# Performance work log

Measured on AMD Instinct MI355X. Metric: run time of the kernel, lower is better.

The kernel has to match this reference:

```python
import jax, jax.numpy as jnp
import numpy as np

B, K, E, L, H, ENS = 32768, 5, 16, 128, 3, 3

def setup_inputs() -> dict:
    key = jax.random.key(0)
    ks = jax.random.split(key, 16)
    w = lambda i, shape: (jax.random.normal(ks[i], shape, jnp.float32) * 0.05)
    return {
        "z": jax.random.normal(ks[0], (B, L), jnp.float32),
        "anchors": jax.random.normal(ks[1], (B, K, 2), jnp.float32),
        # anchor_embed MLP: Linear(2,E) -> ReLU -> Linear(E,E)
        "W1": w(2, (E, 2)), "b1": w(3, (E,)),
        "W2": w(4, (E, E)), "b2": w(5, (E,)),
        # LSTMCell(E, L): gates order i,f,g,o
        "W_ih": w(6, (4 * L, E)), "W_hh": w(7, (4 * L, L)),
        "b_ih": w(8, (4 * L,)), "b_hh": w(9, (4 * L,)),
        # progress head Linear(L,1)
        "Wp": w(10, (1, L)), "bp": w(11, (1,)),
        # risk ensemble: ENS stacked Linear(L,1)
        "Wr": w(12, (ENS, L)), "br": w(13, (ENS,)),
    }

def reference(z, anchors, W1, b1, W2, b2, W_ih, W_hh, b_ih, b_hh, Wp, bp, Wr, br):
    Bc, Kc, _ = anchors.shape
    # anchor embedding MLP (B,K,2) -> (B,K,E)
    emb = jnp.maximum(anchors @ W1.T + b1, 0.0) @ W2.T + b2
    inp = emb.reshape(Bc * Kc, -1)                      # (B*K, E)
    h = jnp.broadcast_to(z[:, None, :], (Bc, Kc, z.shape[-1])).reshape(Bc * Kc, -1)
    c = jnp.zeros_like(h)
    x_proj = inp @ W_ih.T + b_ih                        # input projection constant over steps
    for _ in range(H):  # fixed small rollout horizon
        gates = x_proj + h @ W_hh.T + b_hh              # (B*K, 4L)
        i_g, f_g, g_g, o_g = jnp.split(gates, 4, axis=-1)
        i_g = jax.nn.sigmoid(i_g)
        f_g = jax.nn.sigmoid(f_g)
        g_g = jnp.tanh(g_g)
        o_g = jax.nn.sigmoid(o_g)
        c = f_g * c + i_g * g_g
        h = o_g * jnp.tanh(c)
    h = h.reshape(Bc, Kc, -1)                           # (B,K,L)
    progress = (h @ Wp.T + bp)[..., 0]                  # (B,K)
    risks = jnp.einsum('bkl,el->ebk', h, Wr) + br[:, None, None]  # (ENS,B,K)
    risk_mean = risks.mean(axis=0)
    unc = jnp.var(jax.nn.sigmoid(risks), axis=0, ddof=1)  # torch .var is unbiased
    return risk_mean, progress, unc, risks
```

## Files before the change

kernel.cpp:

```cpp
#include <hip/hip_runtime.h>

#define BN 32768
#define KN 5
#define LN 128
#define HN 3
#define ROWS (BN*KN)
#define BK ROWS
#define MT 64
#define TILES (ROWS/MT)
#define WGS 512
#define TPW (TILES/WGS)
#define THREADS 512
#define ASTR 168
#define LOG2E 1.44269504089f

using bf16x8 = __attribute__((ext_vector_type(8))) __bf16;
using bf16x2 = __attribute__((ext_vector_type(2))) __bf16;
using f32x4  = __attribute__((ext_vector_type(4))) float;
using u16x8  = __attribute__((ext_vector_type(8))) unsigned short;

__device__ inline unsigned short f2bf(float x) {
    union { float f; unsigned u; } v; v.f = x;
    unsigned r = v.u + 0x7FFFu + ((v.u >> 16) & 1u);
    return (unsigned short)(r >> 16);
}
#if __has_builtin(__builtin_amdgcn_cvt_pk_bf16_f32)
__device__ inline unsigned short f2bf_fast(float x) {
    union { bf16x2 v; unsigned short us[2]; } u;
    u.v = __builtin_amdgcn_cvt_pk_bf16_f32(x, x);
    return u.us[0];
}
#else
__device__ inline unsigned short f2bf_fast(float x) { return f2bf(x); }
#endif
__device__ inline float bf2f(unsigned short b) {
    union { unsigned u; float f; } v; v.u = ((unsigned)b) << 16; return v.f;
}
__device__ inline float sigm(float x) {
    return __builtin_amdgcn_rcpf(1.0f + __builtin_amdgcn_exp2f(-LOG2E * x));
}
__device__ inline f32x4 splat4(float x) { f32x4 r; r[0]=x; r[1]=x; r[2]=x; r[3]=x; return r; }

__global__ __launch_bounds__(THREADS, 2)
void wahead_kernel(const float* __restrict__ z,   const float* __restrict__ anchors,
                   const float* __restrict__ W1,  const float* __restrict__ b1,
                   const float* __restrict__ W2,  const float* __restrict__ b2,
                   const float* __restrict__ Wih, const float* __restrict__ Whh,
                   const float* __restrict__ bih, const float* __restrict__ bhh,
                   const float* __restrict__ Wp,  const float* __restrict__ bp,
                   const float* __restrict__ Wr,  const float* __restrict__ br,
                   float* __restrict__ out)
{
    __shared__ unsigned short sA[2 * MT * ASTR];
    __shared__ float sW1[32], sb1[16], sW2[16 * 17], sb2[16], sWp[128], sWr[384];

    const int tid  = threadIdx.x;
    const int wv   = tid >> 6;
    const int lane = tid & 63;
    const int quad = lane >> 4;
    const int cc   = lane & 15;

    if (tid < 32)  sW1[tid] = W1[tid];
    if (tid < 16)  { sb1[tid] = b1[tid]; sb2[tid] = b2[tid]; }
    if (tid < 256) sW2[(tid >> 4) * 17 + (tid & 15)] = W2[tid];
    if (tid < 128) sWp[tid] = Wp[tid];
    if (tid < 384) sWr[tid] = Wr[tid];

    bf16x8 Bf[4][5];
    float  biasv[4];
    #pragma unroll
    for (int t = 0; t < 4; ++t) {
        const float sc = (t == 2) ? (2.0f * LOG2E) : (-LOG2E);
        const int n = t * 128 + wv * 16 + cc;
        biasv[t] = sc * (bih[n] + bhh[n]);
        #pragma unroll
        for (int kt = 0; kt < 5; ++kt) {
            const int k0 = kt * 32 + quad * 8;
            float v[8];
            if (k0 < 16) {
                const float4 p0 = *reinterpret_cast<const float4*>(Wih + n * 16 + k0);
                const float4 p1 = *reinterpret_cast<const float4*>(Wih + n * 16 + k0 + 4);
                v[0]=p0.x; v[1]=p0.y; v[2]=p0.z; v[3]=p0.w;
                v[4]=p1.x; v[5]=p1.y; v[6]=p1.z; v[7]=p1.w;
            } else if (k0 < 144) {
                const float4 p0 = *reinterpret_cast<const float4*>(Whh + n * 128 + (k0 - 16));
                const float4 p1 = *reinterpret_cast<const float4*>(Whh + n * 128 + (k0 - 16) + 4);
                v[0]=p0.x; v[1]=p0.y; v[2]=p0.z; v[3]=p0.w;
                v[4]=p1.x; v[5]=p1.y; v[6]=p1.z; v[7]=p1.w;
            } else {
                #pragma unroll
                for (int j = 0; j < 8; ++j) v[j] = 0.0f;
            }
            union { bf16x8 bv; unsigned short us[8]; } pk;
            #pragma unroll
            for (int j = 0; j < 8; ++j) pk.us[j] = f2bf(sc * v[j]);
            Bf[t][kt] = pk.bv;
        }
    }

    const float bpv = bp[0];
    const float br0 = br[0], br1 = br[1], br2 = br[2];

    __syncthreads();

    const int erow = tid >> 3;
    const int esub = tid & 7;

    #pragma unroll 1
    for (int ti = 0; ti < TPW; ++ti) {
        const int tile = blockIdx.x * TPW + ti;
        const int r0g  = tile * MT;

        {
            const int gr = r0g + erow;
            const float ax = anchors[gr * 2], ay = anchors[gr * 2 + 1];
            const int e0 = esub * 2;
            float a0 = sb2[e0], a1 = sb2[e0 + 1];
            #pragma unroll
            for (int hh = 0; hh < 16; ++hh) {
                float pre = fmaf(sW1[hh * 2], ax, fmaf(sW1[hh * 2 + 1], ay, sb1[hh]));
                pre = fmaxf(pre, 0.0f);
                a0 = fmaf(pre, sW2[e0 * 17 + hh], a0);
                a1 = fmaf(pre, sW2[(e0 + 1) * 17 + hh], a1);
            }
            const unsigned short b0 = f2bf(a0), b1v = f2bf(a1);
            #pragma unroll
            for (int bufi = 0; bufi < 2; ++bufi) {
                unsigned short* row = &sA[bufi * MT * ASTR + erow * ASTR];
                row[e0]       = b0;  row[e0 + 1]       = b1v;
                row[144 + e0] = 0;   row[144 + e0 + 1] = 0;
            }
            const unsigned b_idx = (unsigned)gr / 5u;
            const float4* zp = reinterpret_cast<const float4*>(z + (size_t)b_idx * 128 + esub * 16);
            const float4 z0 = zp[0], z1 = zp[1], z2 = zp[2], z3 = zp[3];
            union { u16x8 v; unsigned short us[8]; } w0, w1;
            w0.us[0]=f2bf(z0.x); w0.us[1]=f2bf(z0.y); w0.us[2]=f2bf(z0.z); w0.us[3]=f2bf(z0.w);
            w0.us[4]=f2bf(z1.x); w0.us[5]=f2bf(z1.y); w0.us[6]=f2bf(z1.z); w0.us[7]=f2bf(z1.w);
            w1.us[0]=f2bf(z2.x); w1.us[1]=f2bf(z2.y); w1.us[2]=f2bf(z2.z); w1.us[3]=f2bf(z2.w);
            w1.us[4]=f2bf(z3.x); w1.us[5]=f2bf(z3.y); w1.us[6]=f2bf(z3.z); w1.us[7]=f2bf(z3.w);
            unsigned short* hrow = &sA[erow * ASTR + 16 + esub * 16];
            *reinterpret_cast<u16x8*>(hrow)     = w0.v;
            *reinterpret_cast<u16x8*>(hrow + 8) = w1.v;
        }

        float cst[16];
        #pragma unroll
        for (int e = 0; e < 16; ++e) cst[e] = 0.0f;

        #pragma unroll
        for (int s = 0; s < HN; ++s) {
            const int cur = s & 1;
            const int nxt = cur ^ 1;
            __syncthreads();

            f32x4 acc[4][4];
            #pragma unroll
            for (int mt = 0; mt < 4; ++mt)
                #pragma unroll
                for (int t = 0; t < 4; ++t)
                    acc[mt][t] = splat4(biasv[t]);

            bf16x8 af[2][5];
            #pragma unroll
            for (int kt = 0; kt < 5; ++kt)
                af[0][kt] = *reinterpret_cast<const bf16x8*>(
                    &sA[cur * MT * ASTR + cc * ASTR + kt * 32 + quad * 8]);
            #pragma unroll
            for (int mt = 0; mt < 4; ++mt) {
                const int pb = mt & 1;
                if (mt < 3) {
                    #pragma unroll
                    for (int kt = 0; kt < 5; ++kt)
                        af[pb ^ 1][kt] = *reinterpret_cast<const bf16x8*>(
                            &sA[cur * MT * ASTR + ((mt + 1) * 16 + cc) * ASTR + kt * 32 + quad * 8]);
                }
                #pragma unroll
                for (int kt = 0; kt < 5; ++kt)
                    #pragma unroll
                    for (int t = 0; t < 4; ++t)
                        acc[mt][t] = __builtin_amdgcn_mfma_f32_16x16x32_bf16(
                            af[pb][kt], Bf[t][kt], acc[mt][t], 0, 0, 0);
            }

            const int lcol = wv * 16 + cc;
            #pragma unroll
            for (int e = 0; e < 16; ++e) {
                const int mt = e >> 2, r = e & 3;
                const float Ei = __builtin_amdgcn_exp2f(acc[mt][0][r]);
                const float Ef = __builtin_amdgcn_exp2f(acc[mt][1][r]);
                const float Eg = __builtin_amdgcn_exp2f(acc[mt][2][r]);
                const float Eo = __builtin_amdgcn_exp2f(acc[mt][3][r]);
                const float t1  = (1.0f + Ei) * (1.0f + Eg);
                const float ef1 = 1.0f + Ef;
                const float t3  = (Eg - 1.0f) * ef1;
                const float num = fmaf(cst[e], t1, t3);
                const float cn  = num * __builtin_amdgcn_rcpf(t1 * ef1);
                cst[e] = cn;
                const float Ec = __builtin_amdgcn_exp2f(2.0f * LOG2E * cn);
                const float hn = (Ec - 1.0f) *
                    __builtin_amdgcn_rcpf((1.0f + Eo) * (1.0f + Ec));
                const int m = mt * 16 + quad * 4 + r;
                sA[nxt * MT * ASTR + m * ASTR + 16 + lcol] = f2bf_fast(hn);
            }
        }

        __syncthreads();

        {
            const int row = tid >> 3;
            const int j   = tid & 7;
            const unsigned short* hrow = &sA[1 * MT * ASTR + row * ASTR + 16 + j * 16];
            const u16x8 h0 = *reinterpret_cast<const u16x8*>(hrow);
            const u16x8 h1 = *reinterpret_cast<const u16x8*>(hrow + 8);
            float p = 0.f, q0 = 0.f, q1 = 0.f, q2 = 0.f;
            #pragma unroll
            for (int u = 0; u < 16; ++u) {
                const int l = j * 16 + u;
                const float hv = bf2f(u < 8 ? h0[u] : h1[u - 8]);
                p  = fmaf(hv, sWp[l], p);
                q0 = fmaf(hv, sWr[l], q0);
                q1 = fmaf(hv, sWr[128 + l], q1);
                q2 = fmaf(hv, sWr[256 + l], q2);
            }
            #pragma unroll
            for (int m = 1; m < 8; m <<= 1) {
                p  += __shfl_xor(p,  m, 64);
                q0 += __shfl_xor(q0, m, 64);
                q1 += __shfl_xor(q1, m, 64);
                q2 += __shfl_xor(q2, m, 64);
            }
            if (j == 0) {
                const int gr = r0g + row;
                const float prog  = p + bpv;
                const float rr0 = q0 + br0, rr1 = q1 + br1, rr2 = q2 + br2;
                const float rmean = (rr0 + rr1 + rr2) * (1.0f / 3.0f);
                const float s0 = sigm(rr0), s1 = sigm(rr1), s2 = sigm(rr2);
                const float sm = (s0 + s1 + s2) * (1.0f / 3.0f);
                const float d0 = s0 - sm, d1 = s1 - sm, d2 = s2 - sm;
                const float unc = (d0 * d0 + d1 * d1 + d2 * d2) * 0.5f;
                out[gr]          = rmean;
                out[BK + gr]     = prog;
                out[2 * BK + gr] = unc;
                out[3 * BK + gr] = rr0;
                out[4 * BK + gr] = rr1;
                out[5 * BK + gr] = rr2;
            }
        }
    }
}

extern "C" void kernel_launch(void* const* d_in, const int* in_sizes, int n_in,
                              void* d_out, int out_size, void* d_ws, size_t ws_size,
                              hipStream_t stream) {
    const float* z       = (const float*)d_in[0];
    const float* anchors = (const float*)d_in[1];
    const float* W1      = (const float*)d_in[2];
    const float* b1      = (const float*)d_in[3];
    const float* W2      = (const float*)d_in[4];
    const float* b2      = (const float*)d_in[5];
    const float* Wih     = (const float*)d_in[6];
    const float* Whh     = (const float*)d_in[7];
    const float* bih     = (const float*)d_in[8];
    const float* bhh     = (const float*)d_in[9];
    const float* Wp      = (const float*)d_in[10];
    const float* bp      = (const float*)d_in[11];
    const float* Wr      = (const float*)d_in[12];
    const float* br      = (const float*)d_in[13];

    hipLaunchKernelGGL(wahead_kernel, dim3(WGS), dim3(THREADS), 0, stream,
                       z, anchors, W1, b1, W2, b2, Wih, Whh, bih, bhh,
                       Wp, bp, Wr, br, (float*)d_out);
}
```

Measured before the change: 213.0 us.

## Split gate GEMM across 16 waves and exchange gates through LDS

Restructures the LSTM tile processing. Tiles shrink to 32 rows and workgroups grow to 1024 threads, and each wave now computes 32 gate columns of one gate type instead of all four gates for 16 columns. Gate pre-activations go through a new LDS buffer so the elementwise cell update can be spread over all threads, with an extra barrier per step. This cuts per-thread register pressure (fewer B fragments and accumulators) to raise parallelism, at the cost of extra LDS traffic, an extra sync per step and a wider shuffle reduction.

```diff
diff --git a/kernel.cpp b/kernel.cpp
--- a/kernel.cpp
+++ b/kernel.cpp
@@ -6,18 +6,20 @@
 #define HN 3
 #define ROWS (BN*KN)
 #define BK ROWS
-#define MT 64
+#define MT 32
 #define TILES (ROWS/MT)
 #define WGS 512
 #define TPW (TILES/WGS)
-#define THREADS 512
+#define THREADS 1024
 #define ASTR 168
+#define GSTR 132
 #define LOG2E 1.44269504089f
 
 using bf16x8 = __attribute__((ext_vector_type(8))) __bf16;
 using bf16x2 = __attribute__((ext_vector_type(2))) __bf16;
 using f32x4  = __attribute__((ext_vector_type(4))) float;
 using u16x8  = __attribute__((ext_vector_type(8))) unsigned short;
+using u16x4  = __attribute__((ext_vector_type(4))) unsigned short;
 
 __device__ inline unsigned short f2bf(float x) {
     union { float f; unsigned u; } v; v.f = x;
@@ -41,7 +43,7 @@
 }
 __device__ inline f32x4 splat4(float x) { f32x4 r; r[0]=x; r[1]=x; r[2]=x; r[3]=x; return r; }
 
-__global__ __launch_bounds__(THREADS, 2)
+__global__ __launch_bounds__(THREADS)
 void wahead_kernel(const float* __restrict__ z,   const float* __restrict__ anchors,
                    const float* __restrict__ W1,  const float* __restrict__ b1,
                    const float* __restrict__ W2,  const float* __restrict__ b2,
@@ -52,13 +54,16 @@
                    float* __restrict__ out)
 {
     __shared__ unsigned short sA[2 * MT * ASTR];
+    __shared__ float sG[4 * MT * GSTR];
     __shared__ float sW1[32], sb1[16], sW2[16 * 17], sb2[16], sWp[128], sWr[384];
 
     const int tid  = threadIdx.x;
-    const int wv   = tid >> 6;
+    const int v    = tid >> 6;
     const int lane = tid & 63;
     const int quad = lane >> 4;
     const int cc   = lane & 15;
+    const int tg   = v >> 2;
+    const int l0   = 32 * (v & 3);
 
     if (tid < 32)  sW1[tid] = W1[tid];
     if (tid < 16)  { sb1[tid] = b1[tid]; sb2[tid] = b2[tid]; }
@@ -66,35 +71,35 @@
     if (tid < 128) sWp[tid] = Wp[tid];
     if (tid < 384) sWr[tid] = Wr[tid];
 
-    bf16x8 Bf[4][5];
-    float  biasv[4];
+    const float sc = (tg == 2) ? (2.0f * LOG2E) : (-LOG2E);
+    bf16x8 Bf[2][5];
+    float  biasv[2];
     #pragma unroll
-    for (int t = 0; t < 4; ++t) {
-        const float sc = (t == 2) ? (2.0f * LOG2E) : (-LOG2E);
-        const int n = t * 128 + wv * 16 + cc;
-        biasv[t] = sc * (bih[n] + bhh[n]);
+    for (int nt = 0; nt < 2; ++nt) {
+        const int n = 32 * v + nt * 16 + cc;
+        biasv[nt] = sc * (bih[n] + bhh[n]);
         #pragma unroll
         for (int kt = 0; kt < 5; ++kt) {
             const int k0 = kt * 32 + quad * 8;
-            float v[8];
+            float w[8];
             if (k0 < 16) {
                 const float4 p0 = *reinterpret_cast<const float4*>(Wih + n * 16 + k0);
                 const float4 p1 = *reinterpret_cast<const float4*>(Wih + n * 16 + k0 + 4);
-                v[0]=p0.x; v[1]=p0.y; v[2]=p0.z; v[3]=p0.w;
-                v[4]=p1.x; v[5]=p1.y; v[6]=p1.z; v[7]=p1.w;
+                w[0]=p0.x; w[1]=p0.y; w[2]=p0.z; w[3]=p0.w;
+                w[4]=p1.x; w[5]=p1.y; w[6]=p1.z; w[7]=p1.w;
             } else if (k0 < 144) {
                 const float4 p0 = *reinterpret_cast<const float4*>(Whh + n * 128 + (k0 - 16));
                 const float4 p1 = *reinterpret_cast<const float4*>(Whh + n * 128 + (k0 - 16) + 4);
-                v[0]=p0.x; v[1]=p0.y; v[2]=p0.z; v[3]=p0.w;
-                v[4]=p1.x; v[5]=p1.y; v[6]=p1.z; v[7]=p1.w;
+                w[0]=p0.x; w[1]=p0.y; w[2]=p0.z; w[3]=p0.w;
+                w[4]=p1.x; w[5]=p1.y; w[6]=p1.z; w[7]=p1.w;
             } else {
                 #pragma unroll
-                for (int j = 0; j < 8; ++j) v[j] = 0.0f;
+                for (int j = 0; j < 8; ++j) w[j] = 0.0f;
             }
             union { bf16x8 bv; unsigned short us[8]; } pk;
             #pragma unroll
-            for (int j = 0; j < 8; ++j) pk.us[j] = f2bf(sc * v[j]);
-            Bf[t][kt] = pk.bv;
+            for (int j = 0; j < 8; ++j) pk.us[j] = f2bf(sc * w[j]);
+            Bf[nt][kt] = pk.bv;
         }
     }
 
@@ -103,8 +108,8 @@
 
     __syncthreads();
 
-    const int erow = tid >> 3;
-    const int esub = tid & 7;
+    const int erow = tid >> 5;
+    const int ej   = tid & 31;
 
     #pragma unroll 1
     for (int ti = 0; ti < TPW; ++ti) {
@@ -113,39 +118,29 @@
 
         {
             const int gr = r0g + erow;
-            const float ax = anchors[gr * 2], ay = anchors[gr * 2 + 1];
-            const int e0 = esub * 2;
-            float a0 = sb2[e0], a1 = sb2[e0 + 1];
-            #pragma unroll
-            for (int hh = 0; hh < 16; ++hh) {
-                float pre = fmaf(sW1[hh * 2], ax, fmaf(sW1[hh * 2 + 1], ay, sb1[hh]));
-                pre = fmaxf(pre, 0.0f);
-                a0 = fmaf(pre, sW2[e0 * 17 + hh], a0);
-                a1 = fmaf(pre, sW2[(e0 + 1) * 17 + hh], a1);
-            }
-            const unsigned short b0 = f2bf(a0), b1v = f2bf(a1);
-            #pragma unroll
-            for (int bufi = 0; bufi < 2; ++bufi) {
-                unsigned short* row = &sA[bufi * MT * ASTR + erow * ASTR];
-                row[e0]       = b0;  row[e0 + 1]       = b1v;
-                row[144 + e0] = 0;   row[144 + e0 + 1] = 0;
+            if (ej < 16) {
+                const float ax = anchors[gr * 2], ay = anchors[gr * 2 + 1];
+                float acc_e = sb2[ej];
+                #pragma unroll
+                for (int hh = 0; hh < 16; ++hh) {
+                    float pre = fmaf(sW1[hh * 2], ax, fmaf(sW1[hh * 2 + 1], ay, sb1[hh]));
+                    pre = fmaxf(pre, 0.0f);
+                    acc_e = fmaf(pre, sW2[ej * 17 + hh], acc_e);
+                }
+                const unsigned short eb = f2bf(acc_e);
+                sA[0 * MT * ASTR + erow * ASTR + ej] = eb;
+                sA[1 * MT * ASTR + erow * ASTR + ej] = eb;
+                sA[0 * MT * ASTR + erow * ASTR + 144 + ej] = 0;
+                sA[1 * MT * ASTR + erow * ASTR + 144 + ej] = 0;
             }
             const unsigned b_idx = (unsigned)gr / 5u;
-            const float4* zp = reinterpret_cast<const float4*>(z + (size_t)b_idx * 128 + esub * 16);
-            const float4 z0 = zp[0], z1 = zp[1], z2 = zp[2], z3 = zp[3];
-            union { u16x8 v; unsigned short us[8]; } w0, w1;
-            w0.us[0]=f2bf(z0.x); w0.us[1]=f2bf(z0.y); w0.us[2]=f2bf(z0.z); w0.us[3]=f2bf(z0.w);
-            w0.us[4]=f2bf(z1.x); w0.us[5]=f2bf(z1.y); w0.us[6]=f2bf(z1.z); w0.us[7]=f2bf(z1.w);
-            w1.us[0]=f2bf(z2.x); w1.us[1]=f2bf(z2.y); w1.us[2]=f2bf(z2.z); w1.us[3]=f2bf(z2.w);
-            w1.us[4]=f2bf(z3.x); w1.us[5]=f2bf(z3.y); w1.us[6]=f2bf(z3.z); w1.us[7]=f2bf(z3.w);
-            unsigned short* hrow = &sA[erow * ASTR + 16 + esub * 16];
-            *reinterpret_cast<u16x8*>(hrow)     = w0.v;
-            *reinterpret_cast<u16x8*>(hrow + 8) = w1.v;
-        }
-
-        float cst[16];
-        #pragma unroll
-        for (int e = 0; e < 16; ++e) cst[e] = 0.0f;
+            const float4 zv = *reinterpret_cast<const float4*>(z + (size_t)b_idx * 128 + ej * 4);
+            union { u16x4 v4; unsigned short us[4]; } zz;
+            zz.us[0]=f2bf(zv.x); zz.us[1]=f2bf(zv.y); zz.us[2]=f2bf(zv.z); zz.us[3]=f2bf(zv.w);
+            *reinterpret_cast<u16x4*>(&sA[erow * ASTR + 16 + ej * 4]) = zz.v4;
+        }
+
+        float cst[4] = {0, 0, 0, 0};
 
         #pragma unroll
         for (int s = 0; s < HN; ++s) {
@@ -153,83 +148,75 @@
             const int nxt = cur ^ 1;
             __syncthreads();
 
-            f32x4 acc[4][4];
-            #pragma unroll
-            for (int mt = 0; mt < 4; ++mt)
-                #pragma unroll
-                for (int t = 0; t < 4; ++t)
-                    acc[mt][t] = splat4(biasv[t]);
-
-            bf16x8 af[2][5];
-            #pragma unroll
-            for (int kt = 0; kt < 5; ++kt)
-                af[0][kt] = *reinterpret_cast<const bf16x8*>(
-                    &sA[cur * MT * ASTR + cc * ASTR + kt * 32 + quad * 8]);
-            #pragma unroll
-            for (int mt = 0; mt < 4; ++mt) {
-                const int pb = mt & 1;
-                if (mt < 3) {
+            #pragma unroll
+            for (int mt = 0; mt < 2; ++mt) {
+                bf16x8 a[5];
+                #pragma unroll
+                for (int kt = 0; kt < 5; ++kt)
+                    a[kt] = *reinterpret_cast<const bf16x8*>(
+                        &sA[cur * MT * ASTR + (mt * 16 + cc) * ASTR + kt * 32 + quad * 8]);
+                #pragma unroll
+                for (int nt = 0; nt < 2; ++nt) {
+                    f32x4 g = splat4(biasv[nt]);
                     #pragma unroll
                     for (int kt = 0; kt < 5; ++kt)
-                        af[pb ^ 1][kt] = *reinterpret_cast<const bf16x8*>(
-                            &sA[cur * MT * ASTR + ((mt + 1) * 16 + cc) * ASTR + kt * 32 + quad * 8]);
+                        g = __builtin_amdgcn_mfma_f32_16x16x32_bf16(a[kt], Bf[nt][kt], g, 0, 0, 0);
+                    const int base = (tg * 32 + mt * 16 + quad * 4) * GSTR + l0 + nt * 16 + cc;
+                    #pragma unroll
+                    for (int r = 0; r < 4; ++r) sG[base + r * GSTR] = g[r];
                 }
-                #pragma unroll
-                for (int kt = 0; kt < 5; ++kt)
-                    #pragma unroll
-                    for (int t = 0; t < 4; ++t)
-                        acc[mt][t] = __builtin_amdgcn_mfma_f32_16x16x32_bf16(
-                            af[pb][kt], Bf[t][kt], acc[mt][t], 0, 0, 0);
-            }
-
-            const int lcol = wv * 16 + cc;
-            #pragma unroll
-            for (int e = 0; e < 16; ++e) {
-                const int mt = e >> 2, r = e & 3;
-                const float Ei = __builtin_amdgcn_exp2f(acc[mt][0][r]);
-                const float Ef = __builtin_amdgcn_exp2f(acc[mt][1][r]);
-                const float Eg = __builtin_amdgcn_exp2f(acc[mt][2][r]);
-                const float Eo = __builtin_amdgcn_exp2f(acc[mt][3][r]);
+            }
+
+            __syncthreads();
+
+            #pragma unroll
+            for (int e = 0; e < 4; ++e) {
+                const int row = 2 * v + (e >> 1);
+                const int l   = lane + 64 * (e & 1);
+                const float gi = sG[(0 * MT + row) * GSTR + l];
+                const float gf = sG[(1 * MT + row) * GSTR + l];
+                const float gg = sG[(2 * MT + row) * GSTR + l];
+                const float go = sG[(3 * MT + row) * GSTR + l];
+                const float Ei = __builtin_amdgcn_exp2f(gi);
+                const float Ef = __builtin_amdgcn_exp2f(gf);
+                const float Eg = __builtin_amdgcn_exp2f(gg);
+                const float Eo = __builtin_amdgcn_exp2f(go);
                 const float t1  = (1.0f + Ei) * (1.0f + Eg);
                 const float ef1 = 1.0f + Ef;
-                const float t3  = (Eg - 1.0f) * ef1;
-                const float num = fmaf(cst[e], t1, t3);
+                const float num = fmaf(cst[e], t1, (Eg - 1.0f) * ef1);
                 const float cn  = num * __builtin_amdgcn_rcpf(t1 * ef1);
                 cst[e] = cn;
                 const float Ec = __builtin_amdgcn_exp2f(2.0f * LOG2E * cn);
                 const float hn = (Ec - 1.0f) *
                     __builtin_amdgcn_rcpf((1.0f + Eo) * (1.0f + Ec));
-                const int m = mt * 16 + quad * 4 + r;
-                sA[nxt * MT * ASTR + m * ASTR + 16 + lcol] = f2bf_fast(hn);
+                sA[nxt * MT * ASTR + row * ASTR + 16 + l] = f2bf_fast(hn);
             }
         }
 
         __syncthreads();
 
         {
-            const int row = tid >> 3;
-            const int j   = tid & 7;
-            const unsigned short* hrow = &sA[1 * MT * ASTR + row * ASTR + 16 + j * 16];
-            const u16x8 h0 = *reinterpret_cast<const u16x8*>(hrow);
-            const u16x8 h1 = *reinterpret_cast<const u16x8*>(hrow + 8);
+            const int row = erow;
+            const u16x4 hv4 = *reinterpret_cast<const u16x4*>(
+                &sA[1 * MT * ASTR + row * ASTR + 16 + ej * 4]);
             float p = 0.f, q0 = 0.f, q1 = 0.f, q2 = 0.f;
             #pragma unroll
-            for (int u = 0; u < 16; ++u) {
-                const int l = j * 16 + u;
-                const float hv = bf2f(u < 8 ? h0[u] : h1[u - 8]);
+            for (int u = 0; u < 4; ++u) {
+                const int l = ej * 4 + u;
+                const float hv = bf2f(hv4[u]);
                 p  = fmaf(hv, sWp[l], p);
                 q0 = fmaf(hv, sWr[l], q0);
                 q1 = fmaf(hv, sWr[128 + l], q1);
                 q2 = fmaf(hv, sWr[256 + l], q2);
             }
             #pragma unroll
-            for (int m = 1; m < 8; m <<= 1) {
+            for (int m = 1; m < 32; m <<= 1) {
                 p  += __shfl_xor(p,  m, 64);
                 q0 += __shfl_xor(q0, m, 64);
                 q1 += __shfl_xor(q1, m, 64);
                 q2 += __shfl_xor(q2, m, 64);
             }
-            if (j == 0) {
+            if (ej == 0) {
                 const int gr = r0g + row;
                 const float prog  = p + bpv;
                 const float rr0 = q0 + br0, rr1 = q1 + br1, rr2 = q2 + br2;
@@ -248,6 +235,7 @@
         }
     }
 }
+
 
 extern "C" void kernel_launch(void* const* d_in, const int* in_sizes, int n_in,
                               void* d_out, int out_size, void* d_ws, size_t ws_size,
```

Measured after the change: 279.7 us. 1.31x slower.

## Split tiles into two half-pipelines interleaving MFMA with LSTM pointwise and epilogue

Applied to the files above, without the earlier changes.

Each 64-row tile is split into two 32-row halves that run software-pipelined. The MFMA gate product for one half is issued while the exp/rcp pointwise LSTM update of the other half runs, so the matrix and transcendental units can overlap. The final hidden state goes to a separate LDS buffer, which lets the previous tile's head and epilogue run during the next tile's first step. The cost is extra barriers per tile, more LDS, and higher register pressure from two live accumulator sets.

```diff
diff --git a/kernel.cpp b/kernel.cpp
--- a/kernel.cpp
+++ b/kernel.cpp
@@ -12,6 +12,7 @@
 #define TPW (TILES/WGS)
 #define THREADS 512
 #define ASTR 168
+#define FSTR 136
 #define LOG2E 1.44269504089f
 
 using bf16x8 = __attribute__((ext_vector_type(8))) __bf16;
@@ -52,6 +53,7 @@
                    float* __restrict__ out)
 {
     __shared__ unsigned short sA[2 * MT * ASTR];
+    __shared__ unsigned short sF[MT * FSTR];
     __shared__ float sW1[32], sb1[16], sW2[16 * 17], sb2[16], sWp[128], sWr[384];
 
     const int tid  = threadIdx.x;
@@ -101,152 +103,173 @@
     const float bpv = bp[0];
     const float br0 = br[0], br1 = br[1], br2 = br[2];
 
+    f32x4 acc0[2][4], acc1[2][4];
+    float cst0[8], cst1[8];
+
+    auto do_mfma = [&](f32x4 (&acc)[2][4], int pipe, int buf) {
+        #pragma unroll
+        for (int mt = 0; mt < 2; ++mt)
+            #pragma unroll
+            for (int t = 0; t < 4; ++t) acc[mt][t] = splat4(biasv[t]);
+        #pragma unroll
+        for (int mt = 0; mt < 2; ++mt) {
+            const int row = pipe * 32 + mt * 16 + cc;
+            bf16x8 a[5];
+            #pragma unroll
+            for (int kt = 0; kt < 5; ++kt)
+                a[kt] = *reinterpret_cast<const bf16x8*>(
+                    &sA[buf * MT * ASTR + row * ASTR + kt * 32 + quad * 8]);
+            #pragma unroll
+            for (int kt = 0; kt < 5; ++kt)
+                #pragma unroll
+                for (int t = 0; t < 4; ++t)
+                    acc[mt][t] = __builtin_amdgcn_mfma_f32_16x16x32_bf16(
+                        a[kt], Bf[t][kt], acc[mt][t], 0, 0, 0);
+        }
+    };
+
+    auto do_pw = [&](f32x4 (&acc)[2][4], float (&cst)[8], int pipe, int dstbuf,
+                     bool final_h) {
+        const int lcol = wv * 16 + cc;
+        #pragma unroll
+        for (int e = 0; e < 8; ++e) {
+            const int mt = e >> 2, r = e & 3;
+            const float Ei = __builtin_amdgcn_exp2f(acc[mt][0][r]);
+            const float Ef = __builtin_amdgcn_exp2f(acc[mt][1][r]);
+            const float Eg = __builtin_amdgcn_exp2f(acc[mt][2][r]);
+            const float Eo = __builtin_amdgcn_exp2f(acc[mt][3][r]);
+            const float t1  = (1.0f + Ei) * (1.0f + Eg);
+            const float ef1 = 1.0f + Ef;
+            const float num = fmaf(cst[e], t1, (Eg - 1.0f) * ef1);
+            const float cn  = num * __builtin_amdgcn_rcpf(t1 * ef1);
+            cst[e] = cn;
+            const float Ec = __builtin_amdgcn_exp2f(2.0f * LOG2E * cn);
+            const float hn = (Ec - 1.0f) *
+                __builtin_amdgcn_rcpf((1.0f + Eo) * (1.0f + Ec));
+            const int m = pipe * 32 + mt * 16 + quad * 4 + r;
+            if (final_h) sF[m * FSTR + lcol] = f2bf_fast(hn);
+            else         sA[dstbuf * MT * ASTR + m * ASTR + 16 + lcol] = f2bf_fast(hn);
+        }
+    };
+
+    auto do_stage = [&](int r0g) {
+        const int erow = tid >> 3, esub = tid & 7;
+        const int gr = r0g + erow;
+        const float ax = anchors[gr * 2], ay = anchors[gr * 2 + 1];
+        const unsigned b_idx = (unsigned)gr / 5u;
+        const float4* zp = reinterpret_cast<const float4*>(z + (size_t)b_idx * 128 + esub * 16);
+        const float4 z0 = zp[0], z1 = zp[1], z2 = zp[2], z3 = zp[3];
+        const int e0 = esub * 2;
+        float a0 = sb2[e0], a1 = sb2[e0 + 1];
+        #pragma unroll
+        for (int hh = 0; hh < 16; ++hh) {
+            float pre = fmaf(sW1[hh * 2], ax, fmaf(sW1[hh * 2 + 1], ay, sb1[hh]));
+            pre = fmaxf(pre, 0.0f);
+            a0 = fmaf(pre, sW2[e0 * 17 + hh], a0);
+            a1 = fmaf(pre, sW2[(e0 + 1) * 17 + hh], a1);
+        }
+        const unsigned short b0 = f2bf(a0), b1v = f2bf(a1);
+        #pragma unroll
+        for (int bufi = 0; bufi < 2; ++bufi) {
+            unsigned short* row = &sA[bufi * MT * ASTR + erow * ASTR];
+            row[e0]       = b0;  row[e0 + 1]       = b1v;
+            row[144 + e0] = 0;   row[144 + e0 + 1] = 0;
+        }
+        union { u16x8 v; unsigned short us[8]; } w0, w1;
+        w0.us[0]=f2bf(z0.x); w0.us[1]=f2bf(z0.y); w0.us[2]=f2bf(z0.z); w0.us[3]=f2bf(z0.w);
+        w0.us[4]=f2bf(z1.x); w0.us[5]=f2bf(z1.y); w0.us[6]=f2bf(z1.z); w0.us[7]=f2bf(z1.w);
+        w1.us[0]=f2bf(z2.x); w1.us[1]=f2bf(z2.y); w1.us[2]=f2bf(z2.z); w1.us[3]=f2bf(z2.w);
+        w1.us[4]=f2bf(z3.x); w1.us[5]=f2bf(z3.y); w1.us[6]=f2bf(z3.z); w1.us[7]=f2bf(z3.w);
+        unsigned short* hrow = &sA[erow * ASTR + 16 + esub * 16];
+        *reinterpret_cast<u16x8*>(hrow)     = w0.v;
+        *reinterpret_cast<u16x8*>(hrow + 8) = w1.v;
+    };
+
+    auto do_epi = [&](int r0g) {
+        const int row = tid >> 3, j = tid & 7;
+        const unsigned short* hrow = &sF[row * FSTR + j * 16];
+        const u16x8 h0 = *reinterpret_cast<const u16x8*>(hrow);
+        const u16x8 h1 = *reinterpret_cast<const u16x8*>(hrow + 8);
+        float p = 0.f, q0 = 0.f, q1 = 0.f, q2 = 0.f;
+        #pragma unroll
+        for (int u = 0; u < 16; ++u) {
+            const int l = j * 16 + u;
+            const float hv = bf2f(u < 8 ? h0[u] : h1[u - 8]);
+            p  = fmaf(hv, sWp[l], p);
+            q0 = fmaf(hv, sWr[l], q0);
+            q1 = fmaf(hv, sWr[128 + l], q1);
+            q2 = fmaf(hv, sWr[256 + l], q2);
+        }
+        #pragma unroll
+        for (int m = 1; m < 8; m <<= 1) {
+            p  += __shfl_xor(p,  m, 64);
+            q0 += __shfl_xor(q0, m, 64);
+            q1 += __shfl_xor(q1, m, 64);
+            q2 += __shfl_xor(q2, m, 64);
+        }
+        if (j == 0) {
+            const int gr = r0g + row;
+            const float prog  = p + bpv;
+            const float rr0 = q0 + br0, rr1 = q1 + br1, rr2 = q2 + br2;
+            const float rmean = (rr0 + rr1 + rr2) * (1.0f / 3.0f);
+            const float s0 = sigm(rr0), s1 = sigm(rr1), s2 = sigm(rr2);
+            const float sm = (s0 + s1 + s2) * (1.0f / 3.0f);
+            const float d0 = s0 - sm, d1 = s1 - sm, d2 = s2 - sm;
+            const float unc = (d0 * d0 + d1 * d1 + d2 * d2) * 0.5f;
+            out[gr]          = rmean;
+            out[BK + gr]     = prog;
+            out[2 * BK + gr] = unc;
+            out[3 * BK + gr] = rr0;
+            out[4 * BK + gr] = rr1;
+            out[5 * BK + gr] = rr2;
+        }
+    };
+
     __syncthreads();
 
-    const int erow = tid >> 3;
-    const int esub = tid & 7;
+    int prev_r0g = 0;
+    bool have_prev = false;
 
     #pragma unroll 1
     for (int ti = 0; ti < TPW; ++ti) {
-        const int tile = blockIdx.x * TPW + ti;
-        const int r0g  = tile * MT;
-
-        {
-            const int gr = r0g + erow;
-            const float ax = anchors[gr * 2], ay = anchors[gr * 2 + 1];
-            const int e0 = esub * 2;
-            float a0 = sb2[e0], a1 = sb2[e0 + 1];
-            #pragma unroll
-            for (int hh = 0; hh < 16; ++hh) {
-                float pre = fmaf(sW1[hh * 2], ax, fmaf(sW1[hh * 2 + 1], ay, sb1[hh]));
-                pre = fmaxf(pre, 0.0f);
-                a0 = fmaf(pre, sW2[e0 * 17 + hh], a0);
-                a1 = fmaf(pre, sW2[(e0 + 1) * 17 + hh], a1);
-            }
-            const unsigned short b0 = f2bf(a0), b1v = f2bf(a1);
-            #pragma unroll
-            for (int bufi = 0; bufi < 2; ++bufi) {
-                unsigned short* row = &sA[bufi * MT * ASTR + erow * ASTR];
-                row[e0]       = b0;  row[e0 + 1]       = b1v;
-                row[144 + e0] = 0;   row[144 + e0 + 1] = 0;
-            }
-            const unsigned b_idx = (unsigned)gr / 5u;
-            const float4* zp = reinterpret_cast<const float4*>(z + (size_t)b_idx * 128 + esub * 16);
-            const float4 z0 = zp[0], z1 = zp[1], z2 = zp[2], z3 = zp[3];
-            union { u16x8 v; unsigned short us[8]; } w0, w1;
-            w0.us[0]=f2bf(z0.x); w0.us[1]=f2bf(z0.y); w0.us[2]=f2bf(z0.z); w0.us[3]=f2bf(z0.w);
-            w0.us[4]=f2bf(z1.x); w0.us[5]=f2bf(z1.y); w0.us[6]=f2bf(z1.z); w0.us[7]=f2bf(z1.w);
-            w1.us[0]=f2bf(z2.x); w1.us[1]=f2bf(z2.y); w1.us[2]=f2bf(z2.z); w1.us[3]=f2bf(z2.w);
-            w1.us[4]=f2bf(z3.x); w1.us[5]=f2bf(z3.y); w1.us[6]=f2bf(z3.z); w1.us[7]=f2bf(z3.w);
-            unsigned short* hrow = &sA[erow * ASTR + 16 + esub * 16];
-            *reinterpret_cast<u16x8*>(hrow)     = w0.v;
-            *reinterpret_cast<u16x8*>(hrow + 8) = w1.v;
-        }
-
-        float cst[16];
-        #pragma unroll
-        for (int e = 0; e < 16; ++e) cst[e] = 0.0f;
-
-        #pragma unroll
-        for (int s = 0; s < HN; ++s) {
-            const int cur = s & 1;
-            const int nxt = cur ^ 1;
-            __syncthreads();
-
-            f32x4 acc[4][4];
-            #pragma unroll
-            for (int mt = 0; mt < 4; ++mt)
-                #pragma unroll
-                for (int t = 0; t < 4; ++t)
-                    acc[mt][t] = splat4(biasv[t]);
-
-            bf16x8 af[2][5];
-            #pragma unroll
-            for (int kt = 0; kt < 5; ++kt)
-                af[0][kt] = *reinterpret_cast<const bf16x8*>(
-                    &sA[cur * MT * ASTR + cc * ASTR + kt * 32 + quad * 8]);
-            #pragma unroll
-            for (int mt = 0; mt < 4; ++mt) {
-                const int pb = mt & 1;
-                if (mt < 3) {
-                    #pragma unroll
-                    for (int kt = 0; kt < 5; ++kt)
-                        af[pb ^ 1][kt] = *reinterpret_cast<const bf16x8*>(
-                            &sA[cur * MT * ASTR + ((mt + 1) * 16 + cc) * ASTR + kt * 32 + quad * 8]);
-                }
-                #pragma unroll
-                for (int kt = 0; kt < 5; ++kt)
-                    #pragma unroll
-                    for (int t = 0; t < 4; ++t)
-                        acc[mt][t] = __builtin_amdgcn_mfma_f32_16x16x32_bf16(
-                            af[pb][kt], Bf[t][kt], acc[mt][t], 0, 0, 0);
-            }
-
-            const int lcol = wv * 16 + cc;
-            #pragma unroll
-            for (int e = 0; e < 16; ++e) {
-                const int mt = e >> 2, r = e & 3;
-                const float Ei = __builtin_amdgcn_exp2f(acc[mt][0][r]);
-                const float Ef = __builtin_amdgcn_exp2f(acc[mt][1][r]);
-                const float Eg = __builtin_amdgcn_exp2f(acc[mt][2][r]);
-                const float Eo = __builtin_amdgcn_exp2f(acc[mt][3][r]);
-                const float t1  = (1.0f + Ei) * (1.0f + Eg);
-                const float ef1 = 1.0f + Ef;
-                const float t3  = (Eg - 1.0f) * ef1;
-                const float num = fmaf(cst[e], t1, t3);
-                const float cn  = num * __builtin_amdgcn_rcpf(t1 * ef1);
-                cst[e] = cn;
-                const float Ec = __builtin_amdgcn_exp2f(2.0f * LOG2E * cn);
-                const float hn = (Ec - 1.0f) *
-                    __builtin_amdgcn_rcpf((1.0f + Eo) * (1.0f + Ec));
-                const int m = mt * 16 + quad * 4 + r;
-                sA[nxt * MT * ASTR + m * ASTR + 16 + lcol] = f2bf_fast(hn);
-            }
-        }
-
-        __syncthreads();
-
-        {
-            const int row = tid >> 3;
-            const int j   = tid & 7;
-            const unsigned short* hrow = &sA[1 * MT * ASTR + row * ASTR + 16 + j * 16];
-            const u16x8 h0 = *reinterpret_cast<const u16x8*>(hrow);
-            const u16x8 h1 = *reinterpret_cast<const u16x8*>(hrow + 8);
-            float p = 0.f, q0 = 0.f, q1 = 0.f, q2 = 0.f;
-            #pragma unroll
-            for (int u = 0; u < 16; ++u) {
-                const int l = j * 16 + u;
-                const float hv = bf2f(u < 8 ? h0[u] : h1[u - 8]);
-                p  = fmaf(hv, sWp[l], p);
-                q0 = fmaf(hv, sWr[l], q0);
-                q1 = fmaf(hv, sWr[128 + l], q1);
-                q2 = fmaf(hv, sWr[256 + l], q2);
-            }
-            #pragma unroll
-            for (int m = 1; m < 8; m <<= 1) {
-                p  += __shfl_xor(p,  m, 64);
-                q0 += __shfl_xor(q0, m, 64);
-                q1 += __shfl_xor(q1, m, 64);
-                q2 += __shfl_xor(q2, m, 64);
-            }
-            if (j == 0) {
-                const int gr = r0g + row;
-                const float prog  = p + bpv;
-                const float rr0 = q0 + br0, rr1 = q1 + br1, rr2 = q2 + br2;
-                const float rmean = (rr0 + rr1 + rr2) * (1.0f / 3.0f);
-                const float s0 = sigm(rr0), s1 = sigm(rr1), s2 = sigm(rr2);
-                const float sm = (s0 + s1 + s2) * (1.0f / 3.0f);
-                const float d0 = s0 - sm, d1 = s1 - sm, d2 = s2 - sm;
-                const float unc = (d0 * d0 + d1 * d1 + d2 * d2) * 0.5f;
-                out[gr]          = rmean;
-                out[BK + gr]     = prog;
-                out[2 * BK + gr] = unc;
-                out[3 * BK + gr] = rr0;
-                out[4 * BK + gr] = rr1;
-                out[5 * BK + gr] = rr2;
-            }
-        }
+        const int r0g = (blockIdx.x * TPW + ti) * MT;
+
+        __syncthreads();
+        do_stage(r0g);
+        if (have_prev) do_pw(acc1, cst1, 1, 0, true);
+        #pragma unroll
+        for (int e = 0; e < 8; ++e) { cst0[e] = 0.0f; cst1[e] = 0.0f; }
+
+        __syncthreads();
+        do_mfma(acc0, 0, 0);
+        do_mfma(acc1, 1, 0);
+        if (have_prev) do_epi(prev_r0g);
+        do_pw(acc0, cst0, 0, 1, false);
+
+        __syncthreads();
+        do_mfma(acc0, 0, 1);
+        do_pw(acc1, cst1, 1, 1, false);
+
+        __syncthreads();
+        do_mfma(acc1, 1, 1);
+        do_pw(acc0, cst0, 0, 0, false);
+
+        __syncthreads();
+        do_mfma(acc0, 0, 0);
+        do_pw(acc1, cst1, 1, 0, false);
+
+        __syncthreads();
+        do_mfma(acc1, 1, 0);
+        do_pw(acc0, cst0, 0, 0, true);
+
+        have_prev = true;
+        prev_r0g  = r0g;
     }
+
+    __syncthreads();
+    do_pw(acc1, cst1, 1, 0, true);
+    __syncthreads();
+    do_epi(prev_r0g);
 }
 
 extern "C" void kernel_launch(void* const* d_in, const int* in_sizes, int n_in,
```

Result: no change. 215.9 us (+1.3%).
